# Performance work log

Measured on AMD Instinct MI355X. Metric: run time of the kernel, lower is better.

## Reference

```python
import jax, jax.numpy as jnp
import numpy as np

N, E, C, H, DH, NB, NA, FC = 30000, 480000, 128, 8, 16, 32, 16, 64
AH = H * DH  # 128 = attn-heads feature dim = mul_alpha


def smooth_leaky_relu(x, alpha=0.2):
    # Equiformer SmoothLeakyReLU: (1+a)/2 * x + (1-a)/2 * x * (2*sigmoid(x) - 1)
    return 0.5 * (1.0 + alpha) * x + 0.5 * (1.0 - alpha) * x * (2.0 * jax.nn.sigmoid(x) - 1.0)


def setup_inputs() -> dict:
    key = jax.random.key(0)
    ks = jax.random.split(key, 20)

    def rn(k, shape, scale=1.0):
        return jax.random.normal(k, shape, dtype=jnp.float32) * scale

    inp = {
        "node_feats": rn(ks[0], (N, C)),
        "node_attr": rn(ks[1], (N, NA)),
        "edge_attr": rn(ks[2], (E, 1)),          # scalar spherical-harmonic channel
        "edge_embedding": rn(ks[3], (E, NB)),     # radial basis embedding
        # message_src_proj (bias) / message_dst_proj (no bias)
        "W_src": rn(ks[4], (C, C), 1.0 / np.sqrt(C)),
        "b_src": jnp.zeros((C,), jnp.float32),
        "W_dst": rn(ks[5], (C, C), 1.0 / np.sqrt(C)),
        # radial network (dtp_rad) for external TP weights
        "W_fc1": rn(ks[6], (NB + 2 * NA, FC), 1.0 / np.sqrt(NB + 2 * NA)),
        "b_fc1": jnp.zeros((FC,), jnp.float32),
        "W_fc2": rn(ks[7], (FC, FC), 1.0 / np.sqrt(FC)),
        "b_fc2": jnp.zeros((FC,), jnp.float32),
        "W_fc3": rn(ks[8], (FC, C), 1.0 / np.sqrt(FC)),
        # attention_score_net
        "W_alpha": rn(ks[9], (C, AH), 1.0 / np.sqrt(C)),
        # edge_message_net.lin (followed by gate)
        "W_lin": rn(ks[10], (C, C), 1.0 / np.sqrt(C)),
        # value_net internal depthwise-TP weights + its linear
        "w_int": rn(ks[11], (C,)),
        "W_val": rn(ks[12], (C, AH), 1.0 / np.sqrt(C)),
        # attention_dot [num_heads, mul_alpha_head]
        "att_dot": rn(ks[13], (H, DH), 1.0 / np.sqrt(DH)),
        # output projection
        "W_out": rn(ks[14], (AH, C), 1.0 / np.sqrt(AH)),
        "b_out": jnp.zeros((C,), jnp.float32),
        "edge_src": jax.random.randint(ks[15], (E,), 0, N),
        "edge_dst": jax.random.randint(ks[16], (E,), 0, N),
    }
    return inp


def reference(node_feats, node_attr, edge_attr, edge_embedding,
              W_src, b_src, W_dst,
              W_fc1, b_fc1, W_fc2, b_fc2, W_fc3,
              W_alpha, W_lin, w_int, W_val, att_dot, W_out, b_out,
              edge_src, edge_dst):
    # node projections then gather to edges
    msg_src = node_feats @ W_src + b_src
    msg_dst = node_feats @ W_dst
    message = msg_src[edge_src] + msg_dst[edge_dst]                    # [E, C]

    # radial net on concat(edge_embedding, src_attr, dst_attr)
    wf = jnp.concatenate([edge_embedding, node_attr[edge_src], node_attr[edge_dst]], axis=-1)
    h = jax.nn.silu(wf @ W_fc1 + b_fc1)
    h = jax.nn.silu(h @ W_fc2 + b_fc2)
    weight = h @ W_fc3                                                 # [E, C] depthwise-TP weights

    # depthwise tensor product with scalar edge_attr, radial-weighted
    message = message * edge_attr * weight                             # [E, C]

    # attention scores -> heads
    scores = (message @ W_alpha).reshape(E, H, DH)                     # [E, H, DH]

    # value path: lin + gate (SiLU on scalars), internal-weight dtp, lin -> heads
    value = jax.nn.silu(message @ W_lin)                               # [E, C]
    value = value * edge_attr * w_int                                  # [E, C]
    value = (value @ W_val).reshape(E, H, DH)                          # [E, H, DH]

    scores = smooth_leaky_relu(scores)
    logits = jnp.einsum('ehk,hk->eh', scores, att_dot)                 # [E, H]

    # segment softmax over destination nodes (torch_geometric.utils.softmax)
    m = jax.ops.segment_max(logits, edge_dst, num_segments=N)          # [N, H]
    m = jnp.where(jnp.isfinite(m), m, 0.0)
    ex = jnp.exp(logits - m[edge_dst])
    den = jax.ops.segment_sum(ex, edge_dst, num_segments=N)
    alpha = ex / (den[edge_dst] + 1e-16)                               # [E, H]

    # attention-weighted scatter-add aggregation
    out = jax.ops.segment_sum(value * alpha[:, :, None], edge_dst, num_segments=N)  # [N, H, DH]
    out = out.reshape(N, AH)
    return out @ W_out + b_out                                         # [N, C]
```

## Files before the change

kernel.cpp:

```cpp
#include <hip/hip_runtime.h>
#include <hip/hip_bf16.h>
#include <cstdint>
#include <cstddef>


typedef unsigned short u16;
typedef unsigned int u32;
typedef __attribute__((ext_vector_type(8))) short bf16x8;
typedef __attribute__((ext_vector_type(4))) float f32x4;

union fu_ { float f; u32 u; };
static __device__ __forceinline__ float lo2f(u32 v) { fu_ x; x.u = v << 16; return x.f; }
static __device__ __forceinline__ float hi2f(u32 v) { fu_ x; x.u = v & 0xFFFF0000u; return x.f; }
static __device__ __forceinline__ u16 f2bf(float f) {
    union { __hip_bfloat16 h; u16 u; } c;
    c.h = __float2bfloat16(f);
    return c.u;
}
static __device__ __forceinline__ u32 pack2(float a, float b) {
    return (u32)f2bf(a) | ((u32)f2bf(b) << 16);
}
static __device__ __forceinline__ float sigmoidf_(float x) { return 1.0f / (1.0f + __expf(-x)); }
static __device__ __forceinline__ float siluf_(float x)    { return x * sigmoidf_(x); }
static __device__ __forceinline__ float slreluf_(float x)  { return x * (0.2f + 0.8f * sigmoidf_(x)); }

#define MFMA16(a, b, c) __builtin_amdgcn_mfma_f32_16x16x32_bf16((a), (b), (c), 0, 0, 0)

static __device__ __forceinline__ bf16x8 ld8f_bf(const float* __restrict__ p) {
    const float4 x = *reinterpret_cast<const float4*>(p);
    const float4 y = *reinterpret_cast<const float4*>(p + 4);
    bf16x8 r;
    r[0] = (short)f2bf(x.x); r[1] = (short)f2bf(x.y);
    r[2] = (short)f2bf(x.z); r[3] = (short)f2bf(x.w);
    r[4] = (short)f2bf(y.x); r[5] = (short)f2bf(y.y);
    r[6] = (short)f2bf(y.z); r[7] = (short)f2bf(y.w);
    return r;
}

__global__ void hist_k(const int* __restrict__ dst, int* __restrict__ deg, int E) {
    int i = blockIdx.x * blockDim.x + threadIdx.x;
    if (i < E) atomicAdd(&deg[dst[i]], 1);
}

__global__ void scan_k(const int* __restrict__ deg, int* __restrict__ rowptr,
                       int* __restrict__ cursor, int n) {
    __shared__ int part[1024];
    const int t = threadIdx.x;
    const int C = (n + 1023) / 1024;
    const int lo = t * C;
    const int hi = (lo + C < n) ? (lo + C) : n;
    int s = 0;
    for (int i = lo; i < hi; ++i) s += deg[i];
    part[t] = s;
    __syncthreads();
    for (int off = 1; off < 1024; off <<= 1) {
        int v = part[t];
        int u = (t >= off) ? part[t - off] : 0;
        __syncthreads();
        part[t] = v + u;
        __syncthreads();
    }
    int excl = (t == 0) ? 0 : part[t - 1];
    for (int i = lo; i < hi; ++i) {
        rowptr[i] = excl;
        cursor[i] = excl;
        excl += deg[i];
    }
    if (t == 1023) rowptr[n] = part[1023];
}

__global__ void fill_k(const int* __restrict__ dst, int* __restrict__ cursor,
                       int* __restrict__ pos, int E) {
    int i = blockIdx.x * blockDim.x + threadIdx.x;
    if (i < E) {
        int d = dst[i];
        int p = atomicAdd(&cursor[d], 1);
        pos[i] = p;
    }
}

__global__ void prep_w_k(const float* __restrict__ Wa, const float* __restrict__ Wl,
                         const float* __restrict__ Wv,
                         const float* __restrict__ W1, const float* __restrict__ W2,
                         const float* __restrict__ W3,
                         const float* __restrict__ Wsrc, const float* __restrict__ Wdst,
                         const float* __restrict__ Wout,
                         u16* __restrict__ Wct, u16* __restrict__ Wvt,
                         u16* __restrict__ Bt1, u16* __restrict__ Bt2,
                         u16* __restrict__ Bt3,
                         u16* __restrict__ Wst, u16* __restrict__ Wdt,
                         u16* __restrict__ Wot) {
    int idx = blockIdx.x * 256 + threadIdx.x;
    if (idx < 32768) {
        int c = idx >> 7, k = idx & 127;
        float v = (c < 128) ? Wa[(size_t)k * 128 + c] : Wl[(size_t)k * 128 + (c - 128)];
        Wct[idx] = f2bf(v);
    } else if (idx < 49152) {
        int t = idx - 32768;
        int j = t >> 7, c = t & 127;
        Wvt[t] = f2bf(Wv[(size_t)c * 128 + j]);
    } else if (idx < 53248) {
        int t = idx - 49152;
        int c = t >> 6, k = t & 63;
        Bt1[t] = f2bf(W1[(size_t)k * 64 + c]);
    } else if (idx < 57344) {
        int t = idx - 53248;
        int c = t >> 6, k = t & 63;
        Bt2[t] = f2bf(W2[(size_t)k * 64 + c]);
    } else if (idx < 65536) {
        int t = idx - 57344;
        int c = t >> 6, k = t & 63;
        Bt3[t] = f2bf(W3[(size_t)k * 128 + c]);
    } else if (idx < 81920) {
        int t = idx - 65536;
        int c = t >> 7, k = t & 127;
        Wst[t] = f2bf(Wsrc[(size_t)k * 128 + c]);
    } else if (idx < 98304) {
        int t = idx - 81920;
        int c = t >> 7, k = t & 127;
        Wdt[t] = f2bf(Wdst[(size_t)k * 128 + c]);
    } else if (idx < 114688) {
        int t = idx - 98304;
        int c = t >> 7, k = t & 127;
        Wot[t] = f2bf(Wout[(size_t)k * 128 + c]);
    }
}

__global__ __launch_bounds__(256) void proj_mfma_k(const float* __restrict__ A,
                                                   const u16* __restrict__ Wt,
                                                   const float* __restrict__ bias,
                                                   float* __restrict__ Out, int M) {
    const int tid  = threadIdx.x;
    const int lane = tid & 63;
    const int w    = tid >> 6;
    const int lr   = lane & 15;
    const int lg   = lane >> 4;
    const int e0   = blockIdx.x * 64;

    f32x4 acc[4][2];
#pragma unroll
    for (int m = 0; m < 4; ++m)
#pragma unroll
        for (int n = 0; n < 2; ++n) acc[m][n] = (f32x4)(0.0f);

#pragma unroll
    for (int ks = 0; ks < 4; ++ks) {
        const int kk = lg * 8 + ks * 32;
        bf16x8 a[4], b[2];
#pragma unroll
        for (int m = 0; m < 4; ++m) {
            int row = e0 + lr + 16 * m;
            row = (row < M) ? row : (M - 1);
            a[m] = ld8f_bf(&A[(size_t)row * 128 + kk]);
        }
#pragma unroll
        for (int n = 0; n < 2; ++n) {
            const int c = 32 * w + 16 * n + lr;
            b[n] = *reinterpret_cast<const bf16x8*>(&Wt[(size_t)c * 128 + kk]);
        }
#pragma unroll
        for (int m = 0; m < 4; ++m)
#pragma unroll
            for (int n = 0; n < 2; ++n) acc[m][n] = MFMA16(a[m], b[n], acc[m][n]);
    }

#pragma unroll
    for (int n = 0; n < 2; ++n) {
        const int j = 32 * w + 16 * n + lr;
        const float bv = bias ? bias[j] : 0.0f;
#pragma unroll
        for (int m = 0; m < 4; ++m)
#pragma unroll
            for (int i = 0; i < 4; ++i) {
                const int row = e0 + 16 * m + 4 * lg + i;
                if (row < M) Out[(size_t)row * 128 + j] = acc[m][n][i] + bv;
            }
    }
}

__global__ __launch_bounds__(256, 3) void msg_attn_k(
    const float* __restrict__ eemb, const float* __restrict__ nattr,
    const float* __restrict__ ea,
    const int* __restrict__ src, const int* __restrict__ dst,
    const int* __restrict__ pos,
    const u16* __restrict__ Bt1, const float* __restrict__ b1,
    const u16* __restrict__ Bt2, const float* __restrict__ b2,
    const u16* __restrict__ Bt3,
    const float* __restrict__ Ps, const float* __restrict__ Pd,
    const u16* __restrict__ Wct, const u16* __restrict__ Wvt,
    const float* __restrict__ att_dot, const float* __restrict__ w_int,
    float* __restrict__ LG, u16* __restrict__ V, int E) {
    __shared__ __align__(16) char smem[34816];
    char* regA  = smem;
    char* regB  = smem + 16384;
    float* lgs  = (float*)(smem + 32768);

    const int tid  = threadIdx.x;
    const int lane = tid & 63;
    const int w    = tid >> 6;
    const int lr   = lane & 15;
    const int lg   = lane >> 4;
    const int e0   = blockIdx.x * 64;

    {
        f32x4 acc1[4];
#pragma unroll
        for (int m = 0; m < 4; ++m) acc1[m] = (f32x4)(0.0f);
#pragma unroll
        for (int ks = 0; ks < 2; ++ks) {
            const int kk = lg * 8 + ks * 32;
            bf16x8 a[4];
#pragma unroll
            for (int m = 0; m < 4; ++m) {
                int row = e0 + lr + 16 * m;
                row = (row < E) ? row : (E - 1);
                const float* ap;
                if (kk < 32)      ap = &eemb[(size_t)row * 32 + kk];
                else if (kk < 48) ap = &nattr[(size_t)src[row] * 16 + (kk - 32)];
                else              ap = &nattr[(size_t)dst[row] * 16 + (kk - 48)];
                a[m] = ld8f_bf(ap);
            }
            const bf16x8 b = *reinterpret_cast<const bf16x8*>(&Bt1[(size_t)(16 * w + lr) * 64 + kk]);
#pragma unroll
            for (int m = 0; m < 4; ++m) acc1[m] = MFMA16(a[m], b, acc1[m]);
        }
        const int c = 16 * w + lr;
        const float bias = b1[c];
#pragma unroll
        for (int m = 0; m < 4; ++m)
#pragma unroll
            for (int i = 0; i < 4; ++i) {
                const int r = 16 * m + 4 * lg + i;
                const int byte = (r * 128 + c * 2) ^ ((r & 7) << 4);
                *reinterpret_cast<u16*>(regA + byte) = f2bf(siluf_(acc1[m][i] + bias));
            }
    }
    __syncthreads();

    {
        f32x4 acc2[4];
#pragma unroll
        for (int m = 0; m < 4; ++m) acc2[m] = (f32x4)(0.0f);
#pragma unroll
        for (int ks = 0; ks < 2; ++ks) {
            const int kk = lg * 8 + ks * 32;
            bf16x8 a[4];
#pragma unroll
            for (int m = 0; m < 4; ++m) {
                const int r = lr + 16 * m;
                const int byte = (r * 128 + kk * 2) ^ ((r & 7) << 4);
                a[m] = *reinterpret_cast<const bf16x8*>(regA + byte);
            }
            const bf16x8 b = *reinterpret_cast<const bf16x8*>(&Bt2[(size_t)(16 * w + lr) * 64 + kk]);
#pragma unroll
            for (int m = 0; m < 4; ++m) acc2[m] = MFMA16(a[m], b, acc2[m]);
        }
        const int c = 16 * w + lr;
        const float bias = b2[c];
#pragma unroll
        for (int m = 0; m < 4; ++m)
#pragma unroll
            for (int i = 0; i < 4; ++i) {
                const int r = 16 * m + 4 * lg + i;
                const int byte = (r * 128 + c * 2) ^ ((r & 7) << 4);
                *reinterpret_cast<u16*>(regA + 8192 + byte) = f2bf(siluf_(acc2[m][i] + bias));
            }
    }
    __syncthreads();

    {
        f32x4 acc3[2][4];
#pragma unroll
        for (int n = 0; n < 2; ++n)
#pragma unroll
            for (int m = 0; m < 4; ++m) acc3[n][m] = (f32x4)(0.0f);
#pragma unroll
        for (int ks = 0; ks < 2; ++ks) {
            const int kk = lg * 8 + ks * 32;
            bf16x8 a[4];
#pragma unroll
            for (int m = 0; m < 4; ++m) {
                const int r = lr + 16 * m;
                const int byte = (r * 128 + kk * 2) ^ ((r & 7) << 4);
                a[m] = *reinterpret_cast<const bf16x8*>(regA + 8192 + byte);
            }
            bf16x8 b[2];
#pragma unroll
            for (int n = 0; n < 2; ++n) {
                const int c = 32 * w + 16 * n + lr;
                b[n] = *reinterpret_cast<const bf16x8*>(&Bt3[(size_t)c * 64 + kk]);
            }
#pragma unroll
            for (int n = 0; n < 2; ++n)
#pragma unroll
                for (int m = 0; m < 4; ++m) acc3[n][m] = MFMA16(a[m], b[n], acc3[n][m]);
        }
#pragma unroll
        for (int n = 0; n < 2; ++n) {
            const int c = 32 * w + 16 * n + lr;
#pragma unroll
            for (int m = 0; m < 4; ++m)
#pragma unroll
                for (int i = 0; i < 4; ++i) {
                    const int r = 16 * m + 4 * lg + i;
                    const int byte = (r * 256 + c * 2) ^ ((r & 7) << 4);
                    *reinterpret_cast<u16*>(regB + byte) = f2bf(acc3[n][m][i]);
                }
        }
    }
    __syncthreads();

#pragma unroll
    for (int t = 0; t < 4; ++t) {
        const int idx = tid + 256 * t;
        const int r = idx >> 4;
        const int c8 = (idx & 15) * 8;
        const int row = e0 + r;
        if (row >= E) continue;
        const int byte = (r * 256 + c8 * 2) ^ ((r & 7) << 4);
        const uint4 wv = *reinterpret_cast<const uint4*>(regB + byte);
        const float wt[8] = {lo2f(wv.x), hi2f(wv.x), lo2f(wv.y), hi2f(wv.y),
                             lo2f(wv.z), hi2f(wv.z), lo2f(wv.w), hi2f(wv.w)};
        const int s = src[row], d = dst[row];
        const float eav = ea[row];
        const float4 ps0 = *reinterpret_cast<const float4*>(&Ps[(size_t)s * 128 + c8]);
        const float4 ps1 = *reinterpret_cast<const float4*>(&Ps[(size_t)s * 128 + c8 + 4]);
        const float4 pd0 = *reinterpret_cast<const float4*>(&Pd[(size_t)d * 128 + c8]);
        const float4 pd1 = *reinterpret_cast<const float4*>(&Pd[(size_t)d * 128 + c8 + 4]);
        float m[8];
        m[0] = (ps0.x + pd0.x) * eav * wt[0];
        m[1] = (ps0.y + pd0.y) * eav * wt[1];
        m[2] = (ps0.z + pd0.z) * eav * wt[2];
        m[3] = (ps0.w + pd0.w) * eav * wt[3];
        m[4] = (ps1.x + pd1.x) * eav * wt[4];
        m[5] = (ps1.y + pd1.y) * eav * wt[5];
        m[6] = (ps1.z + pd1.z) * eav * wt[6];
        m[7] = (ps1.w + pd1.w) * eav * wt[7];
        u32 p0 = pack2(m[0], m[1]), p1 = pack2(m[2], m[3]);
        u32 p2 = pack2(m[4], m[5]), p3 = pack2(m[6], m[7]);
        *reinterpret_cast<uint4*>(regB + byte) = make_uint4(p0, p1, p2, p3);
    }
    __syncthreads();

    const int c0w = w * 64;
    float eav_r[4];
    if (w >= 2) {
#pragma unroll
        for (int i = 0; i < 4; ++i) eav_r[i] = ea[e0 + 16 * 0 + 4 * lg + i];
    }
#pragma unroll
    for (int n = 0; n < 4; ++n) {
        f32x4 accn[4];
#pragma unroll
        for (int m = 0; m < 4; ++m) accn[m] = (f32x4)(0.0f);
#pragma unroll
        for (int ks = 0; ks < 4; ++ks) {
            const int kk = lg * 8 + ks * 32;
            const bf16x8 b = *reinterpret_cast<const bf16x8*>(
                &Wct[(size_t)(c0w + 16 * n + lr) * 128 + kk]);
#pragma unroll
            for (int m = 0; m < 4; ++m) {
                const int r = lr + 16 * m;
                const int byte = (r * 256 + kk * 2) ^ ((r & 7) << 4);
                const bf16x8 am = *reinterpret_cast<const bf16x8*>(regB + byte);
                accn[m] = MFMA16(am, b, accn[m]);
            }
        }
        if (w < 2) {
            const float ad = att_dot[c0w + 16 * n + lr];
            const int h = 4 * w + n;
#pragma unroll
            for (int m = 0; m < 4; ++m) {
#pragma unroll
                for (int i = 0; i < 4; ++i) {
                    float s = slreluf_(accn[m][i]) * ad;
                    s += __shfl_xor(s, 1);
                    s += __shfl_xor(s, 2);
                    s += __shfl_xor(s, 4);
                    s += __shfl_xor(s, 8);
                    if (lr == 0) lgs[(16 * m + 4 * lg + i) * 8 + h] = s;
                }
            }
        } else {
            const int cc = 64 * (w - 2) + 16 * n + lr;
            const float wi = w_int[cc];
#pragma unroll
            for (int m = 0; m < 4; ++m) {
#pragma unroll
                for (int i = 0; i < 4; ++i) {
                    const int r = 16 * m + 4 * lg + i;
                    int row = e0 + r;
                    row = (row < E) ? row : (E - 1);
                    const float v1 = siluf_(accn[m][i]) * ea[row] * wi;
                    const int byte = (r * 256 + cc * 2) ^ ((r & 7) << 4);
                    *reinterpret_cast<u16*>(regA + byte) = f2bf(v1);
                }
            }
        }
    }
    __syncthreads();

    {
        f32x4 acc2[4][2];
#pragma unroll
        for (int m = 0; m < 4; ++m)
#pragma unroll
            for (int n = 0; n < 2; ++n) acc2[m][n] = (f32x4)(0.0f);
#pragma unroll
        for (int ks = 0; ks < 4; ++ks) {
            const int kk = lg * 8 + ks * 32;
            bf16x8 a2[4], b2[2];
#pragma unroll
            for (int m = 0; m < 4; ++m) {
                const int r = lr + 16 * m;
                const int byte = (r * 256 + kk * 2) ^ ((r & 7) << 4);
                a2[m] = *reinterpret_cast<const bf16x8*>(regA + byte);
            }
#pragma unroll
            for (int n = 0; n < 2; ++n) {
                const int j = 32 * w + 16 * n + lr;
                b2[n] = *reinterpret_cast<const bf16x8*>(&Wvt[(size_t)j * 128 + kk]);
            }
#pragma unroll
            for (int m = 0; m < 4; ++m)
#pragma unroll
                for (int n = 0; n < 2; ++n) acc2[m][n] = MFMA16(a2[m], b2[n], acc2[m][n]);
        }
        u16* Vout = (u16*)regB;
#pragma unroll
        for (int n = 0; n < 2; ++n) {
            const int j = 32 * w + 16 * n + lr;
#pragma unroll
            for (int m = 0; m < 4; ++m)
#pragma unroll
                for (int i = 0; i < 4; ++i) {
                    const int r = 16 * m + 4 * lg + i;
                    Vout[r * 128 + j] = f2bf(acc2[m][n][i]);
                }
        }
    }
    __syncthreads();

    const uint4* vo = reinterpret_cast<const uint4*>(regB);
#pragma unroll
    for (int t = 0; t < 4; ++t) {
        const int idx = tid + 256 * t;
        const int row = idx >> 4;
        const int c16 = idx & 15;
        if (e0 + row < E) {
            const int p = pos[e0 + row];
            *reinterpret_cast<uint4*>(&V[(size_t)p * 128 + c16 * 8]) = vo[idx];
        }
    }
    if (tid < 128) {
        const int row = tid >> 1;
        if (e0 + row < E) {
            const int p = pos[e0 + row];
            *reinterpret_cast<float4*>(&LG[(size_t)p * 8 + (tid & 1) * 4]) =
                *reinterpret_cast<const float4*>(&lgs[tid * 4]);
        }
    }
}

__global__ __launch_bounds__(256) void aggregate_k(const int* __restrict__ rowptr,
                                                   const float* __restrict__ LG,
                                                   const u16* __restrict__ V,
                                                   float* __restrict__ ACC, int Nn) {
    const int node = blockIdx.x * 4 + (threadIdx.x >> 6);
    const int lane = threadIdx.x & 63;
    if (node >= Nn) return;
    const int s = rowptr[node], t = rowptr[node + 1];
    const int h = lane >> 3;
    float a0 = 0.0f, a1 = 0.0f, ds = 0.0f;
    for (int i = s; i < t; ++i) {
        const float exv = __expf(LG[(size_t)i * 8 + h]);
        const u32 vv = *reinterpret_cast<const u32*>(&V[(size_t)i * 128 + lane * 2]);
        a0 += exv * lo2f(vv);
        a1 += exv * hi2f(vv);
        ds += exv;
    }
    const float inv = 1.0f / (ds + 1e-16f);
    ACC[(size_t)node * 128 + lane * 2]     = a0 * inv;
    ACC[(size_t)node * 128 + lane * 2 + 1] = a1 * inv;
}

extern "C" void kernel_launch(void* const* d_in, const int* in_sizes, int n_in,
                              void* d_out, int out_size, void* d_ws, size_t ws_size,
                              hipStream_t stream) {
    const float* node_feats = (const float*)d_in[0];
    const float* node_attr  = (const float*)d_in[1];
    const float* edge_attr  = (const float*)d_in[2];
    const float* edge_emb   = (const float*)d_in[3];
    const float* W_src      = (const float*)d_in[4];
    const float* b_src      = (const float*)d_in[5];
    const float* W_dst      = (const float*)d_in[6];
    const float* W_fc1      = (const float*)d_in[7];
    const float* b_fc1      = (const float*)d_in[8];
    const float* W_fc2      = (const float*)d_in[9];
    const float* b_fc2      = (const float*)d_in[10];
    const float* W_fc3      = (const float*)d_in[11];
    const float* W_alpha    = (const float*)d_in[12];
    const float* W_lin      = (const float*)d_in[13];
    const float* w_int      = (const float*)d_in[14];
    const float* W_val      = (const float*)d_in[15];
    const float* att_dot    = (const float*)d_in[16];
    const float* W_out      = (const float*)d_in[17];
    const float* b_out      = (const float*)d_in[18];
    const int* esrc         = (const int*)d_in[19];
    const int* edst         = (const int*)d_in[20];

    const int Nn = in_sizes[0] / 128;
    const int E  = in_sizes[19];

    char* w = (char*)d_ws;
    auto alloc = [&](size_t bytes) {
        char* p = w;
        w += (bytes + 255) & ~(size_t)255;
        return p;
    };
    u16* V      = (u16*)alloc((size_t)E * 128 * 2);
    float* LG   = (float*)alloc((size_t)E * 8 * 4);
    float* Psrc = (float*)alloc((size_t)Nn * 128 * 4);
    float* ACC  = Psrc;
    float* Pdst = (float*)alloc((size_t)Nn * 128 * 4);
    int* deg    = (int*)alloc((size_t)Nn * 4);
    int* rowptr = (int*)alloc((size_t)(Nn + 1) * 4);
    int* cursor = (int*)alloc((size_t)Nn * 4);
    int* pos    = (int*)alloc((size_t)E * 4);
    u16* Wct    = (u16*)alloc(32768 * 2);
    u16* Wvt    = (u16*)alloc(16384 * 2);
    u16* Bt1    = (u16*)alloc(4096 * 2);
    u16* Bt2    = (u16*)alloc(4096 * 2);
    u16* Bt3    = (u16*)alloc(8192 * 2);
    u16* Wst    = (u16*)alloc(16384 * 2);
    u16* Wdt    = (u16*)alloc(16384 * 2);
    u16* Wot    = (u16*)alloc(16384 * 2);

    hipMemsetAsync(deg, 0, (size_t)Nn * 4, stream);
    hist_k<<<(E + 255) / 256, 256, 0, stream>>>(edst, deg, E);
    scan_k<<<1, 1024, 0, stream>>>(deg, rowptr, cursor, Nn);
    fill_k<<<(E + 255) / 256, 256, 0, stream>>>(edst, cursor, pos, E);
    prep_w_k<<<448, 256, 0, stream>>>(W_alpha, W_lin, W_val, W_fc1, W_fc2, W_fc3,
                                      W_src, W_dst, W_out,
                                      Wct, Wvt, Bt1, Bt2, Bt3, Wst, Wdt, Wot);

    const int nb_node = (Nn + 63) / 64;
    const int nb_e    = (E + 63) / 64;

    proj_mfma_k<<<nb_node, 256, 0, stream>>>(node_feats, Wst, b_src, Psrc, Nn);
    proj_mfma_k<<<nb_node, 256, 0, stream>>>(node_feats, Wdt, nullptr, Pdst, Nn);

    msg_attn_k<<<nb_e, 256, 0, stream>>>(edge_emb, node_attr, edge_attr, esrc, edst, pos,
                                         Bt1, b_fc1, Bt2, b_fc2, Bt3,
                                         Psrc, Pdst, Wct, Wvt, att_dot, w_int,
                                         LG, V, E);

    aggregate_k<<<(Nn + 3) / 4, 256, 0, stream>>>(rowptr, LG, V, ACC, Nn);

    proj_mfma_k<<<nb_node, 256, 0, stream>>>(ACC, Wot, b_out, (float*)d_out, Nn);
}
```

Before: 523.0 us.

## Process edges in destination-sorted order via gather instead of scattered writes

The counting-sort fill now produces an inverse permutation (sorted slot to edge id) instead of a per-edge position. The message kernel walks edges in dst-sorted order, gathering edge inputs through the permutation and caching src/dst/edge_attr in shared memory, so the V and logit outputs are written contiguously. Consecutive edges in a block now share destination nodes, which should improve locality for the Pd and node_attr gathers. In exchange, edge_embedding and source-side reads become scattered gathers rather than streaming loads.

```diff
diff --git a/kernel.cpp b/kernel.cpp
--- a/kernel.cpp
+++ b/kernel.cpp
@@ -70,12 +70,12 @@
 }
 
 __global__ void fill_k(const int* __restrict__ dst, int* __restrict__ cursor,
-                       int* __restrict__ pos, int E) {
+                       int* __restrict__ eids, int E) {
     int i = blockIdx.x * blockDim.x + threadIdx.x;
     if (i < E) {
         int d = dst[i];
         int p = atomicAdd(&cursor[d], 1);
-        pos[i] = p;
+        eids[p] = i;
     }
 }
 
@@ -182,7 +182,7 @@
     const float* __restrict__ eemb, const float* __restrict__ nattr,
     const float* __restrict__ ea,
     const int* __restrict__ src, const int* __restrict__ dst,
-    const int* __restrict__ pos,
+    const int* __restrict__ eids,
     const u16* __restrict__ Bt1, const float* __restrict__ b1,
     const u16* __restrict__ Bt2, const float* __restrict__ b2,
     const u16* __restrict__ Bt3,
@@ -190,10 +190,14 @@
     const u16* __restrict__ Wct, const u16* __restrict__ Wvt,
     const float* __restrict__ att_dot, const float* __restrict__ w_int,
     float* __restrict__ LG, u16* __restrict__ V, int E) {
-    __shared__ __align__(16) char smem[34816];
-    char* regA  = smem;
-    char* regB  = smem + 16384;
-    float* lgs  = (float*)(smem + 32768);
+    __shared__ __align__(16) char smem[35840];
+    char* regA   = smem;
+    char* regB   = smem + 16384;
+    float* lgs   = (float*)(smem + 32768);
+    int*   eid_l = (int*)(smem + 34816);
+    int*   src_l = eid_l + 64;
+    int*   dst_l = src_l + 64;
+    float* ea_l  = (float*)(dst_l + 64);
 
     const int tid  = threadIdx.x;
     const int lane = tid & 63;
@@ -202,6 +206,16 @@
     const int lg   = lane >> 4;
     const int e0   = blockIdx.x * 64;
 
+    if (tid < 64) {
+        int slot = e0 + tid;
+        int e = (slot < E) ? eids[slot] : eids[E - 1];
+        eid_l[tid] = e;
+        src_l[tid] = src[e];
+        dst_l[tid] = dst[e];
+        ea_l[tid]  = ea[e];
+    }
+    __syncthreads();
+
     {
         f32x4 acc1[4];
 #pragma unroll
@@ -212,12 +226,11 @@
             bf16x8 a[4];
 #pragma unroll
             for (int m = 0; m < 4; ++m) {
-                int row = e0 + lr + 16 * m;
-                row = (row < E) ? row : (E - 1);
+                const int r = lr + 16 * m;
                 const float* ap;
-                if (kk < 32)      ap = &eemb[(size_t)row * 32 + kk];
-                else if (kk < 48) ap = &nattr[(size_t)src[row] * 16 + (kk - 32)];
-                else              ap = &nattr[(size_t)dst[row] * 16 + (kk - 48)];
+                if (kk < 32)      ap = &eemb[(size_t)eid_l[r] * 32 + kk];
+                else if (kk < 48) ap = &nattr[(size_t)src_l[r] * 16 + (kk - 32)];
+                else              ap = &nattr[(size_t)dst_l[r] * 16 + (kk - 48)];
                 a[m] = ld8f_bf(ap);
             }
             const bf16x8 b = *reinterpret_cast<const bf16x8*>(&Bt1[(size_t)(16 * w + lr) * 64 + kk]);
@@ -315,14 +328,13 @@
         const int idx = tid + 256 * t;
         const int r = idx >> 4;
         const int c8 = (idx & 15) * 8;
-        const int row = e0 + r;
-        if (row >= E) continue;
+        if (e0 + r >= E) continue;
         const int byte = (r * 256 + c8 * 2) ^ ((r & 7) << 4);
         const uint4 wv = *reinterpret_cast<const uint4*>(regB + byte);
         const float wt[8] = {lo2f(wv.x), hi2f(wv.x), lo2f(wv.y), hi2f(wv.y),
                              lo2f(wv.z), hi2f(wv.z), lo2f(wv.w), hi2f(wv.w)};
-        const int s = src[row], d = dst[row];
-        const float eav = ea[row];
+        const int s = src_l[r], d = dst_l[r];
+        const float eav = ea_l[r];
         const float4 ps0 = *reinterpret_cast<const float4*>(&Ps[(size_t)s * 128 + c8]);
         const float4 ps1 = *reinterpret_cast<const float4*>(&Ps[(size_t)s * 128 + c8 + 4]);
         const float4 pd0 = *reinterpret_cast<const float4*>(&Pd[(size_t)d * 128 + c8]);
@@ -343,11 +355,6 @@
     __syncthreads();
 
     const int c0w = w * 64;
-    float eav_r[4];
-    if (w >= 2) {
-#pragma unroll
-        for (int i = 0; i < 4; ++i) eav_r[i] = ea[e0 + 16 * 0 + 4 * lg + i];
-    }
 #pragma unroll
     for (int n = 0; n < 4; ++n) {
         f32x4 accn[4];
@@ -389,9 +396,7 @@
 #pragma unroll
                 for (int i = 0; i < 4; ++i) {
                     const int r = 16 * m + 4 * lg + i;
-                    int row = e0 + r;
-                    row = (row < E) ? row : (E - 1);
-                    const float v1 = siluf_(accn[m][i]) * ea[row] * wi;
+                    const float v1 = siluf_(accn[m][i]) * ea_l[r] * wi;
                     const int byte = (r * 256 + cc * 2) ^ ((r & 7) << 4);
                     *reinterpret_cast<u16*>(regA + byte) = f2bf(v1);
                 }
@@ -446,19 +451,14 @@
     for (int t = 0; t < 4; ++t) {
         const int idx = tid + 256 * t;
         const int row = idx >> 4;
-        const int c16 = idx & 15;
-        if (e0 + row < E) {
-            const int p = pos[e0 + row];
-            *reinterpret_cast<uint4*>(&V[(size_t)p * 128 + c16 * 8]) = vo[idx];
-        }
+        if (e0 + row < E)
+            *reinterpret_cast<uint4*>(&V[(size_t)e0 * 128 + idx * 8]) = vo[idx];
     }
     if (tid < 128) {
         const int row = tid >> 1;
-        if (e0 + row < E) {
-            const int p = pos[e0 + row];
-            *reinterpret_cast<float4*>(&LG[(size_t)p * 8 + (tid & 1) * 4]) =
+        if (e0 + row < E)
+            *reinterpret_cast<float4*>(&LG[(size_t)e0 * 8 + tid * 4]) =
                 *reinterpret_cast<const float4*>(&lgs[tid * 4]);
-        }
     }
 }
 
@@ -526,7 +526,7 @@
     int* deg    = (int*)alloc((size_t)Nn * 4);
     int* rowptr = (int*)alloc((size_t)(Nn + 1) * 4);
     int* cursor = (int*)alloc((size_t)Nn * 4);
-    int* pos    = (int*)alloc((size_t)E * 4);
+    int* eids   = (int*)alloc((size_t)E * 4);
     u16* Wct    = (u16*)alloc(32768 * 2);
     u16* Wvt    = (u16*)alloc(16384 * 2);
     u16* Bt1    = (u16*)alloc(4096 * 2);
@@ -539,7 +539,7 @@
     hipMemsetAsync(deg, 0, (size_t)Nn * 4, stream);
     hist_k<<<(E + 255) / 256, 256, 0, stream>>>(edst, deg, E);
     scan_k<<<1, 1024, 0, stream>>>(deg, rowptr, cursor, Nn);
-    fill_k<<<(E + 255) / 256, 256, 0, stream>>>(edst, cursor, pos, E);
+    fill_k<<<(E + 255) / 256, 256, 0, stream>>>(edst, cursor, eids, E);
     prep_w_k<<<448, 256, 0, stream>>>(W_alpha, W_lin, W_val, W_fc1, W_fc2, W_fc3,
                                       W_src, W_dst, W_out,
                                       Wct, Wvt, Bt1, Bt2, Bt3, Wst, Wdt, Wot);
@@ -550,7 +550,7 @@
     proj_mfma_k<<<nb_node, 256, 0, stream>>>(node_feats, Wst, b_src, Psrc, Nn);
     proj_mfma_k<<<nb_node, 256, 0, stream>>>(node_feats, Wdt, nullptr, Pdst, Nn);
 
-    msg_attn_k<<<nb_e, 256, 0, stream>>>(edge_emb, node_attr, edge_attr, esrc, edst, pos,
+    msg_attn_k<<<nb_e, 256, 0, stream>>>(edge_emb, node_attr, edge_attr, esrc, edst, eids,
                                          Bt1, b_fc1, Bt2, b_fc2, Bt3,
                                          Psrc, Pdst, Wct, Wvt, att_dot, w_int,
                                          LG, V, E);
```

New measurement: 499.2 us. 1.05x faster.
